# Kernel optimization log

Hardware: AMD Instinct MI355X
Metric: run time of the kernel (lower is better)

Reference implementation:

```python
import jax, jax.numpy as jnp
import numpy as np

T, B, IN, OUT, N_MODULES, K = 2048, 8, 1024, 1024, 16, 2


def setup_inputs() -> dict:
    key = jax.random.key(0)
    k1, k2, k3 = jax.random.split(key, 3)
    x = jax.random.normal(k1, (T, B, IN), dtype=jnp.float32)          # time-major input
    selection = jax.random.randint(k2, (B, K), 0, N_MODULES, dtype=jnp.int32)
    # kaiming-uniform-ish scale for [n_modules, out, in] weight
    bound = 1.0 / np.sqrt(IN)
    weight = jax.random.uniform(k3, (N_MODULES, OUT, IN), dtype=jnp.float32,
                                minval=-bound, maxval=bound)
    return {"x": x, "selection": selection, "weight": weight}


def reference(x, selection, weight):
    # Faithful to ModularLinear.forward with time_major=True, sum_outputs=False, bias=None.
    # Original computes o = x @ all-expert weights -> [B, n_modules, T, out], then for each
    # selection column i gathers o[b, selection[b, i]] and concats on the last dim.
    # Equivalent math: gather the selected expert weights per (batch, slot) and do one GEMM.
    # x: [T, B, in]; selection: [B, K]; weight: [n_modules, out, in]
    w_sel = weight[selection]                              # [B, K, out, in]
    o = jnp.einsum('tbi,bkoi->tbko', x, w_sel)             # [T, B, K, out]
    t, b, k, d = o.shape
    return o.reshape(t, b, k * d)                          # [T, B, K*out]
```

## Files before the change

kernel.cpp:

```cpp
#include <hip/hip_runtime.h>

#define T_DIM   2048
#define B_DIM   8
#define IN_DIM  1024
#define OUT_DIM 1024
#define NMOD    16
#define KSLOT   2

#define BM 128
#define BN 128
#define BK 32

typedef __bf16 bf16x8 __attribute__((ext_vector_type(8)));
typedef float  f32x4  __attribute__((ext_vector_type(4)));
typedef unsigned short ushort8 __attribute__((ext_vector_type(8)));

typedef const __attribute__((address_space(1))) void* gptr_t;
typedef __attribute__((address_space(3))) void* lptr_t;

__device__ __forceinline__ void async_load16(const void* gp, void* lp) {
  __builtin_amdgcn_global_load_lds((gptr_t)gp, (lptr_t)lp, 16, 0, 0);
}

__device__ __forceinline__ unsigned short f2bf_rne(float f) {
  unsigned int u = __float_as_uint(f);
  u += 0x7fffu + ((u >> 16) & 1u);
  return (unsigned short)(u >> 16);
}

__global__ __launch_bounds__(256) void convert_bf16(
    const float* __restrict__ x, const float* __restrict__ w,
    unsigned short* __restrict__ xb, unsigned short* __restrict__ wb) {
  const long tid = (long)blockIdx.x * blockDim.x + threadIdx.x;
  const long XV = (long)T_DIM * B_DIM * IN_DIM / 8;
  const float4* src;
  unsigned short* dst;
  long v;
  if (tid < XV) { v = tid;      src = (const float4*)x; dst = xb; }
  else          { v = tid - XV; src = (const float4*)w; dst = wb; }
  float4 a = src[2 * v];
  float4 c = src[2 * v + 1];
  ushort8 o;
  o[0] = f2bf_rne(a.x); o[1] = f2bf_rne(a.y); o[2] = f2bf_rne(a.z); o[3] = f2bf_rne(a.w);
  o[4] = f2bf_rne(c.x); o[5] = f2bf_rne(c.y); o[6] = f2bf_rne(c.z); o[7] = f2bf_rne(c.w);
  *(ushort8*)(dst + v * 8) = o;
}

__global__ __launch_bounds__(256) void gemm_mod(
    const unsigned short* __restrict__ xb, const unsigned short* __restrict__ wb,
    const int* __restrict__ sel, float* __restrict__ out) {
  __shared__ alignas(16) unsigned short As[BM * BK];
  __shared__ alignas(16) unsigned short Bs[BN * BK];

  const int nt = blockIdx.x;
  const int mt = blockIdx.y;
  const int bk = blockIdx.z;
  const int b  = bk >> 1;
  const int ks = bk & 1;
  const int expert = sel[bk];

  const int AS = B_DIM * IN_DIM;
  const unsigned short* A  = xb + ((long)mt * BM * B_DIM + b) * IN_DIM;
  const unsigned short* Bw = wb + ((long)expert * OUT_DIM + (long)nt * BN) * IN_DIM;

  const int tid  = threadIdx.x;
  const int lane = tid & 63;
  const int c0 = tid, c1 = tid + 256;

  const int r0 = c0 >> 2, g0 = (c0 & 3) ^ ((r0 >> 2) & 3);
  const int r1 = c1 >> 2, g1 = (c1 & 3) ^ ((r1 >> 2) & 3);
  const long a0 = (long)r0 * AS + g0 * 8;
  const long a1 = (long)r1 * AS + g1 * 8;
  const long b0 = (long)r0 * IN_DIM + g0 * 8;
  const long b1 = (long)r1 * IN_DIM + g1 * 8;

  const int lm = lane & 15;
  const int kg = lane >> 4;
  const int ksw = ((kg ^ ((lm >> 2) & 3))) * 8;

  const int wave = tid >> 6;
  const int wm = (wave >> 1) * 64;
  const int wn = (wave & 1) * 64;

  f32x4 acc[4][4];
  const f32x4 z = {0.f, 0.f, 0.f, 0.f};
  #pragma unroll
  for (int i = 0; i < 4; ++i)
    #pragma unroll
    for (int j = 0; j < 4; ++j) acc[i][j] = z;

  for (int kt = 0; kt < IN_DIM; kt += BK) {
    __syncthreads();
    async_load16(A  + a0 + kt, &As[c0 * 8]);
    async_load16(A  + a1 + kt, &As[c1 * 8]);
    async_load16(Bw + b0 + kt, &Bs[c0 * 8]);
    async_load16(Bw + b1 + kt, &Bs[c1 * 8]);
    __syncthreads();

    bf16x8 af[4], bfr[4];
    #pragma unroll
    for (int mi = 0; mi < 4; ++mi)
      af[mi] = *(const bf16x8*)&As[(wm + mi * 16 + lm) * BK + ksw];
    #pragma unroll
    for (int ni = 0; ni < 4; ++ni)
      bfr[ni] = *(const bf16x8*)&Bs[(wn + ni * 16 + lm) * BK + ksw];

    #pragma unroll
    for (int mi = 0; mi < 4; ++mi)
      #pragma unroll
      for (int ni = 0; ni < 4; ++ni)
        acc[mi][ni] = __builtin_amdgcn_mfma_f32_16x16x32_bf16(af[mi], bfr[ni], acc[mi][ni], 0, 0, 0);
  }

  const int row0 = mt * BM + wm + kg * 4;
  const int col0 = nt * BN + wn + lm;
  #pragma unroll
  for (int mi = 0; mi < 4; ++mi) {
    #pragma unroll
    for (int r = 0; r < 4; ++r) {
      const int t = row0 + mi * 16 + r;
      float* po = out + (long)t * (B_DIM * KSLOT * OUT_DIM)
                      + b * (KSLOT * OUT_DIM) + ks * OUT_DIM + col0;
      #pragma unroll
      for (int ni = 0; ni < 4; ++ni)
        po[ni * 16] = acc[mi][ni][r];
    }
  }
}

extern "C" void kernel_launch(void* const* d_in, const int* in_sizes, int n_in,
                              void* d_out, int out_size, void* d_ws, size_t ws_size,
                              hipStream_t stream) {
  const float* x   = (const float*)d_in[0];
  const int*   sel = (const int*)d_in[1];
  const float* w   = (const float*)d_in[2];
  float* out = (float*)d_out;

  unsigned short* xb = (unsigned short*)d_ws;
  unsigned short* wb = xb + (long)T_DIM * B_DIM * IN_DIM;

  const long total_vecs =
      ((long)T_DIM * B_DIM * IN_DIM + (long)NMOD * OUT_DIM * IN_DIM) / 8;
  dim3 cgrid((unsigned)((total_vecs + 255) / 256));
  convert_bf16<<<cgrid, 256, 0, stream>>>(x, w, xb, wb);

  dim3 ggrid(OUT_DIM / BN, T_DIM / BM, B_DIM * KSLOT);
  gemm_mod<<<ggrid, 256, 0, stream>>>(xb, wb, sel, out);
}
```

Measured before the change: 334.7 us.

## Pre-pack bf16 operands in MFMA fragment order and drop LDS staging

The conversion kernel now writes x and weights in a fragment-major layout, so each lane's 8-element MFMA operand sits contiguously and a wave reads 1KB coalesced per fragment. The GEMM then loads fragments straight from global memory into registers, with no shared-memory staging and no __syncthreads. This removes LDS traffic and the barriers, but gives up sharing within a block: tiles used by several waves are now fetched separately by each wave through the cache. Launch bounds ask for 3 blocks per SIMD and the k-loop is unrolled by 2.

Result: faster. 318.0 us (-5.0%).

```diff
diff --git a/kernel.cpp b/kernel.cpp
--- a/kernel.cpp
+++ b/kernel.cpp
@@ -7,20 +7,9 @@
 #define NMOD    16
 #define KSLOT   2
 
-#define BM 128
-#define BN 128
-#define BK 32
-
 typedef __bf16 bf16x8 __attribute__((ext_vector_type(8)));
 typedef float  f32x4  __attribute__((ext_vector_type(4)));
 typedef unsigned short ushort8 __attribute__((ext_vector_type(8)));
-
-typedef const __attribute__((address_space(1))) void* gptr_t;
-typedef __attribute__((address_space(3))) void* lptr_t;
-
-__device__ __forceinline__ void async_load16(const void* gp, void* lp) {
-  __builtin_amdgcn_global_load_lds((gptr_t)gp, (lptr_t)lp, 16, 0, 0);
-}
 
 __device__ __forceinline__ unsigned short f2bf_rne(float f) {
   unsigned int u = __float_as_uint(f);
@@ -28,59 +17,57 @@
   return (unsigned short)(u >> 16);
 }
 
-__global__ __launch_bounds__(256) void convert_bf16(
+__global__ __launch_bounds__(256) void convert_pack(
     const float* __restrict__ x, const float* __restrict__ w,
-    unsigned short* __restrict__ xb, unsigned short* __restrict__ wb) {
-  const long tid = (long)blockIdx.x * blockDim.x + threadIdx.x;
-  const long XV = (long)T_DIM * B_DIM * IN_DIM / 8;
-  const float4* src;
+    unsigned short* __restrict__ xf, unsigned short* __restrict__ wf) {
+  const int tid = blockIdx.x * blockDim.x + threadIdx.x;
+  const int XV = 1 << 21;
+  const float* src;
   unsigned short* dst;
-  long v;
-  if (tid < XV) { v = tid;      src = (const float4*)x; dst = xb; }
-  else          { v = tid - XV; src = (const float4*)w; dst = wb; }
-  float4 a = src[2 * v];
-  float4 c = src[2 * v + 1];
+  if (tid < XV) {
+    const int v = tid;
+    const int lm = v & 15, kg = (v >> 4) & 127, g = (v >> 11) & 127, b = v >> 18;
+    src = x + (long)(16 * g + lm) * (B_DIM * IN_DIM) + b * IN_DIM + 8 * kg;
+    dst = xf + (long)v * 8;
+  } else {
+    const int v = tid - XV;
+    const int lm = v & 15, kg = (v >> 4) & 127, g = (v >> 11) & 63, e = v >> 17;
+    src = w + (long)e * (OUT_DIM * IN_DIM) + (long)(16 * g + lm) * IN_DIM + 8 * kg;
+    dst = wf + (long)v * 8;
+  }
+  float4 a = ((const float4*)src)[0];
+  float4 c = ((const float4*)src)[1];
   ushort8 o;
   o[0] = f2bf_rne(a.x); o[1] = f2bf_rne(a.y); o[2] = f2bf_rne(a.z); o[3] = f2bf_rne(a.w);
   o[4] = f2bf_rne(c.x); o[5] = f2bf_rne(c.y); o[6] = f2bf_rne(c.z); o[7] = f2bf_rne(c.w);
-  *(ushort8*)(dst + v * 8) = o;
+  *(ushort8*)dst = o;
 }
 
-__global__ __launch_bounds__(256) void gemm_mod(
-    const unsigned short* __restrict__ xb, const unsigned short* __restrict__ wb,
+__global__ __launch_bounds__(256, 3) void gemm_frag(
+    const unsigned short* __restrict__ xf, const unsigned short* __restrict__ wf,
     const int* __restrict__ sel, float* __restrict__ out) {
-  __shared__ alignas(16) unsigned short As[BM * BK];
-  __shared__ alignas(16) unsigned short Bs[BN * BK];
-
   const int nt = blockIdx.x;
   const int mt = blockIdx.y;
   const int bk = blockIdx.z;
   const int b  = bk >> 1;
-  const int ks = bk & 1;
-  const int expert = sel[bk];
-
-  const int AS = B_DIM * IN_DIM;
-  const unsigned short* A  = xb + ((long)mt * BM * B_DIM + b) * IN_DIM;
-  const unsigned short* Bw = wb + ((long)expert * OUT_DIM + (long)nt * BN) * IN_DIM;
+  const int ks_slot = bk & 1;
+  const int e  = sel[bk];
 
   const int tid  = threadIdx.x;
   const int lane = tid & 63;
-  const int c0 = tid, c1 = tid + 256;
-
-  const int r0 = c0 >> 2, g0 = (c0 & 3) ^ ((r0 >> 2) & 3);
-  const int r1 = c1 >> 2, g1 = (c1 & 3) ^ ((r1 >> 2) & 3);
-  const long a0 = (long)r0 * AS + g0 * 8;
-  const long a1 = (long)r1 * AS + g1 * 8;
-  const long b0 = (long)r0 * IN_DIM + g0 * 8;
-  const long b1 = (long)r1 * IN_DIM + g1 * 8;
-
-  const int lm = lane & 15;
-  const int kg = lane >> 4;
-  const int ksw = ((kg ^ ((lm >> 2) & 3))) * 8;
-
   const int wave = tid >> 6;
   const int wm = (wave >> 1) * 64;
   const int wn = (wave & 1) * 64;
+
+  const unsigned short* ap[4];
+  const unsigned short* bp[4];
+  #pragma unroll
+  for (int i = 0; i < 4; ++i) {
+    const int ga = b * 128 + mt * 8 + (wm >> 4) + i;
+    ap[i] = xf + (long)ga * 16384 + lane * 8;
+    const int gb = e * 64 + nt * 8 + (wn >> 4) + i;
+    bp[i] = wf + (long)gb * 16384 + lane * 8;
+  }
 
   f32x4 acc[4][4];
   const f32x4 z = {0.f, 0.f, 0.f, 0.f};
@@ -89,22 +76,14 @@
     #pragma unroll
     for (int j = 0; j < 4; ++j) acc[i][j] = z;
 
-  for (int kt = 0; kt < IN_DIM; kt += BK) {
-    __syncthreads();
-    async_load16(A  + a0 + kt, &As[c0 * 8]);
-    async_load16(A  + a1 + kt, &As[c1 * 8]);
-    async_load16(Bw + b0 + kt, &Bs[c0 * 8]);
-    async_load16(Bw + b1 + kt, &Bs[c1 * 8]);
-    __syncthreads();
-
+  #pragma unroll 2
+  for (int ks = 0; ks < 32; ++ks) {
     bf16x8 af[4], bfr[4];
     #pragma unroll
-    for (int mi = 0; mi < 4; ++mi)
-      af[mi] = *(const bf16x8*)&As[(wm + mi * 16 + lm) * BK + ksw];
-    #pragma unroll
-    for (int ni = 0; ni < 4; ++ni)
-      bfr[ni] = *(const bf16x8*)&Bs[(wn + ni * 16 + lm) * BK + ksw];
-
+    for (int i = 0; i < 4; ++i) {
+      af[i]  = *(const bf16x8*)(ap[i] + ks * 512);
+      bfr[i] = *(const bf16x8*)(bp[i] + ks * 512);
+    }
     #pragma unroll
     for (int mi = 0; mi < 4; ++mi)
       #pragma unroll
@@ -112,15 +91,17 @@
         acc[mi][ni] = __builtin_amdgcn_mfma_f32_16x16x32_bf16(af[mi], bfr[ni], acc[mi][ni], 0, 0, 0);
   }
 
-  const int row0 = mt * BM + wm + kg * 4;
-  const int col0 = nt * BN + wn + lm;
+  const int lm = lane & 15;
+  const int kg = lane >> 4;
+  const int row0 = mt * 128 + wm + kg * 4;
+  const int col0 = nt * 128 + wn + lm;
   #pragma unroll
   for (int mi = 0; mi < 4; ++mi) {
     #pragma unroll
     for (int r = 0; r < 4; ++r) {
       const int t = row0 + mi * 16 + r;
       float* po = out + (long)t * (B_DIM * KSLOT * OUT_DIM)
-                      + b * (KSLOT * OUT_DIM) + ks * OUT_DIM + col0;
+                      + b * (KSLOT * OUT_DIM) + ks_slot * OUT_DIM + col0;
       #pragma unroll
       for (int ni = 0; ni < 4; ++ni)
         po[ni * 16] = acc[mi][ni][r];
@@ -136,14 +117,12 @@
   const float* w   = (const float*)d_in[2];
   float* out = (float*)d_out;
 
-  unsigned short* xb = (unsigned short*)d_ws;
-  unsigned short* wb = xb + (long)T_DIM * B_DIM * IN_DIM;
+  unsigned short* xf = (unsigned short*)d_ws;
+  unsigned short* wf = xf + (long)T_DIM * B_DIM * IN_DIM;
 
-  const long total_vecs =
-      ((long)T_DIM * B_DIM * IN_DIM + (long)NMOD * OUT_DIM * IN_DIM) / 8;
-  dim3 cgrid((unsigned)((total_vecs + 255) / 256));
-  convert_bf16<<<cgrid, 256, 0, stream>>>(x, w, xb, wb);
+  const int total_vecs = (1 << 22);
+  convert_pack<<<dim3(total_vecs / 256), 256, 0, stream>>>(x, w, xf, wf);
 
-  dim3 ggrid(OUT_DIM / BN, T_DIM / BM, B_DIM * KSLOT);
-  gemm_mod<<<ggrid, 256, 0, stream>>>(xb, wb, sel, out);
+  dim3 ggrid(OUT_DIM / 128, T_DIM / 128, B_DIM * KSLOT);
+  gemm_frag<<<ggrid, 256, 0, stream>>>(xf, wf, sel, out);
 }
```
